# Performance work log

Measured on AMD Instinct MI355X. Metric: run time of the kernel, lower is better.

Reference implementation:

```python
import jax, jax.numpy as jnp
import numpy as np

N = 100000      # nodes
F_IN = 512      # num_features
H = 256         # hidden
C = 64          # num_classes
E = 3200000     # edges
K = 10          # APPNP propagation steps
ALPHA = 0.1     # teleport probability


def setup_inputs() -> dict:
    key = jax.random.key(0)
    k_x, k_w0, k_w1, k_e = jax.random.split(key, 4)
    x = jax.random.normal(k_x, (N, F_IN), dtype=jnp.float32)
    w0 = jax.random.normal(k_w0, (F_IN, H), dtype=jnp.float32) / np.sqrt(F_IN).astype(np.float32)
    b0 = jnp.zeros((H,), dtype=jnp.float32)
    w1 = jax.random.normal(k_w1, (H, C), dtype=jnp.float32) / np.sqrt(H).astype(np.float32)
    b1 = jnpps = jnp.zeros((C,), dtype=jnp.float32)
    edge_index = jax.random.randint(k_e, (2, E), 0, N, dtype=jnp.int64)
    return {"x": x, "w0": w0, "b0": b0, "w1": w1, "b1": b1, "edge_index": edge_index}


def _appnp(h, edge_index):
    # Add self loops (PyG APPNP default: gcn_norm with self loops).
    loops = jnp.arange(N, dtype=edge_index.dtype)
    src = jnp.concatenate([edge_index[0], loops])
    dst = jnp.concatenate([edge_index[1], loops])
    # Symmetric GCN normalization: D^{-1/2} (A+I) D^{-1/2}
    deg = jax.ops.segment_sum(jnp.ones_like(src, dtype=h.dtype), dst, num_segments=N)
    dinv = jnp.where(deg > 0, jax.lax.rsqrt(deg), 0.0)
    norm = dinv[src] * dinv[dst]  # [E+N]

    def step(xc, _):
        msg = norm[:, None] * xc[src]                      # gather [E+N, C]
        agg = jax.ops.segment_sum(msg, dst, num_segments=N)  # scatter-add [N, C]
        return (1.0 - ALPHA) * agg + ALPHA * h, None

    out, _ = jax.lax.scan(step, h, None, length=K)
    return out


def reference(x, w0, b0, w1, b1, edge_index):
    # eval mode: dropout is identity
    h = jax.nn.relu(x @ w0 + b0)   # [N, H]
    h = h @ w1 + b1                # [N, C]
    z = _appnp(h, edge_index)      # [N, C]
    return jax.nn.log_softmax(z, axis=1)
```

## Files before the change

kernel.cpp:

```cpp
#include <hip/hip_runtime.h>
#include <hip/hip_bf16.h>

#define NN 100000
#define EE 3200000
#define FIN 512
#define HH 256
#define CC 64
#define KSTEPS 10
#define SB 391
#define NBUC 782
#define EPB 16384
#define NEB 196

typedef __attribute__((ext_vector_type(8))) short bf16x8;
typedef __attribute__((ext_vector_type(8))) short s16x8;
typedef __attribute__((ext_vector_type(4))) float f32x4;
typedef unsigned short ushort_t;

__device__ __forceinline__ short f2bf(float f) {
    union { __hip_bfloat16 h; short s; } u;
    u.h = __float2bfloat16(f);
    return u.s;
}

__device__ __forceinline__ void glds16(const void* g, void* l) {
    __builtin_amdgcn_global_load_lds(
        (const __attribute__((address_space(1))) void*)g,
        (__attribute__((address_space(3))) void*)l, 16, 0, 0);
}

__global__ void prep_w(const float* __restrict__ w0, const float* __restrict__ w1,
                       short* __restrict__ w0t, short* __restrict__ w1t) {
    int t = blockIdx.x * blockDim.x + threadIdx.x;
    if (t < FIN * HH) {
        int k = t >> 8, n = t & 255;
        w0t[n * FIN + k] = f2bf(w0[t]);
    } else if (t < FIN * HH + HH * CC) {
        int u = t - FIN * HH;
        int k = u >> 6, n = u & 63;
        w1t[n * HH + k] = f2bf(w1[u]);
    }
}

__global__ __launch_bounds__(256) void bincnt(const int* __restrict__ ei,
                                              int* __restrict__ bcnt) {
    __shared__ int hb[NBUC];
    int tid = threadIdx.x;
    int base = blockIdx.x * EPB;
    for (int i = tid; i < NBUC; i += 256) hb[i] = 0;
    __syncthreads();
#pragma unroll 4
    for (int i = 0; i < EPB / 256; ++i) {
        int t = base + i * 256 + tid;
        if (t < EE) atomicAdd(&hb[(unsigned)ei[EE + t] >> 7], 1);
    }
    __syncthreads();
    for (int i = tid; i < NBUC; i += 256)
        if (hb[i]) atomicAdd(&bcnt[i], hb[i]);
}

__global__ __launch_bounds__(1024) void bscan(const int* __restrict__ bcnt,
                                              int* __restrict__ eboff) {
    __shared__ int sh[1024];
    int t = threadIdx.x;
    int v = (t < NBUC) ? bcnt[t] : 0;
    sh[t] = v;
    __syncthreads();
    for (int off = 1; off < 1024; off <<= 1) {
        int add = (t >= off) ? sh[t - off] : 0;
        __syncthreads();
        sh[t] += add;
        __syncthreads();
    }
    if (t < NBUC) eboff[t] = sh[t] - v;
}

__global__ __launch_bounds__(256) void binfill(const int* __restrict__ ei,
                                               const int* __restrict__ eboff,
                                               int* __restrict__ bfc,
                                               int* __restrict__ stg) {
    __shared__ int hb[NBUC];
    __shared__ int lb[NBUC];
    int tid = threadIdx.x;
    int base = blockIdx.x * EPB;
    for (int i = tid; i < NBUC; i += 256) hb[i] = 0;
    __syncthreads();
#pragma unroll 4
    for (int i = 0; i < EPB / 256; ++i) {
        int t = base + i * 256 + tid;
        if (t < EE) atomicAdd(&hb[(unsigned)ei[EE + t] >> 7], 1);
    }
    __syncthreads();
    for (int i = tid; i < NBUC; i += 256) {
        int c = hb[i];
        lb[i] = eboff[i] + (c ? atomicAdd(&bfc[i], c) : 0);
        hb[i] = 0;
    }
    __syncthreads();
#pragma unroll 4
    for (int i = 0; i < EPB / 256; ++i) {
        int t = base + i * 256 + tid;
        if (t < EE) {
            int s = ei[t];
            int d = ei[EE + t];
            int b = (unsigned)d >> 7;
            int o = atomicAdd(&hb[b], 1);
            stg[lb[b] + o] = (s << 7) | (d & 127);
        }
    }
}

__global__ __launch_bounds__(256) void bhist(const int* __restrict__ stg,
                                             const int* __restrict__ eboff,
                                             const int* __restrict__ bcnt,
                                             int* __restrict__ cnt) {
    __shared__ int nc[128];
    int b = blockIdx.x, tid = threadIdx.x;
    if (tid < 128) nc[tid] = 0;
    __syncthreads();
    int s0 = eboff[b], n = bcnt[b];
    for (int i = tid; i < n; i += 256) atomicAdd(&nc[stg[s0 + i] & 127], 1);
    __syncthreads();
    int node = b * 128 + tid;
    if (tid < 128 && node < NN) cnt[node] = nc[tid];
}

__global__ __launch_bounds__(256) void deg_kernel(const int* __restrict__ cnt,
                                                  float* __restrict__ dinv,
                                                  float* __restrict__ wco,
                                                  float* __restrict__ sdg,
                                                  int* __restrict__ bsum,
                                                  int* __restrict__ dbc) {
    __shared__ int red[256];
    __shared__ int h[64];
    int tid = threadIdx.x;
    if (tid < 64) h[tid] = 0;
    int i = blockIdx.x * 256 + tid;
    int d = 0, bin = 0;
    if (i < NN) {
        int c = cnt[i];
        d = c + 1;
        bin = min(c, 63);
        float fd = (float)d;
        dinv[i] = rsqrtf(fd);
        wco[i] = 0.9f / fd;
        sdg[i] = sqrtf(fd);
    }
    red[tid] = d;
    __syncthreads();
    if (i < NN) atomicAdd(&h[bin], 1);
    for (int off = 128; off > 0; off >>= 1) {
        if (tid < off) red[tid] += red[tid + off];
        __syncthreads();
    }
    if (tid == 0) bsum[blockIdx.x] = red[0];
    if (tid < 64 && h[tid]) atomicAdd(&dbc[tid], h[tid]);
}

__global__ __launch_bounds__(512) void scanb_kernel(const int* __restrict__ bsum,
                                                    int* __restrict__ boff,
                                                    const int* __restrict__ dbc,
                                                    int* __restrict__ dboff) {
    __shared__ int sh[512];
    int t = threadIdx.x;
    int v = (t < SB) ? bsum[t] : 0;
    sh[t] = v;
    __syncthreads();
    for (int off = 1; off < 512; off <<= 1) {
        int add = (t >= off) ? sh[t - off] : 0;
        __syncthreads();
        sh[t] += add;
        __syncthreads();
    }
    if (t < SB) boff[t] = sh[t] - v;
    __syncthreads();
    int v2 = (t < 64) ? dbc[t] : 0;
    __syncthreads();
    if (t < 64) sh[t] = v2;
    __syncthreads();
    for (int off = 1; off < 64; off <<= 1) {
        int add = (t >= off && t < 64) ? sh[t - off] : 0;
        __syncthreads();
        if (t < 64) sh[t] += add;
        __syncthreads();
    }
    if (t < 64) dboff[t] = sh[t] - v2;
}

__global__ __launch_bounds__(256) void rp_kernel(const int* __restrict__ cnt,
                                                 const int* __restrict__ boff,
                                                 int* __restrict__ rp) {
    __shared__ int sh[256];
    int i = blockIdx.x * 256 + threadIdx.x;
    int d = (i < NN) ? cnt[i] + 1 : 0;
    sh[threadIdx.x] = d;
    __syncthreads();
    for (int off = 1; off < 256; off <<= 1) {
        int add = (threadIdx.x >= off) ? sh[threadIdx.x - off] : 0;
        __syncthreads();
        sh[threadIdx.x] += add;
        __syncthreads();
    }
    int incl = sh[threadIdx.x];
    if (i < NN) rp[i] = boff[blockIdx.x] + incl - d;
    if (i == NN - 1) rp[NN] = boff[blockIdx.x] + incl;
}

__global__ __launch_bounds__(256) void bfill2(const int* __restrict__ stg,
                                              const int* __restrict__ eboff,
                                              const int* __restrict__ bcnt,
                                              const int* __restrict__ rp,
                                              int* __restrict__ eds) {
    __shared__ int nfc[128];
    __shared__ int rpl[129];
    int b = blockIdx.x, tid = threadIdx.x;
    int nodes = min(128, NN - b * 128);
    if (tid < 128) nfc[tid] = 0;
    if (tid <= 128) rpl[tid] = rp[min(b * 128 + tid, NN)];
    __syncthreads();
    int s0 = eboff[b], n = bcnt[b];
    for (int i = tid; i < n; i += 256) {
        int e = stg[s0 + i];
        int loc = e & 127;
        int o = atomicAdd(&nfc[loc], 1);
        eds[rpl[loc] + o] = e >> 7;
    }
    __syncthreads();
    if (tid < nodes) eds[rpl[tid + 1] - 1] = b * 128 + tid;
}

__global__ __launch_bounds__(256) void dperm(const int* __restrict__ cnt,
                                             const int* __restrict__ dboff,
                                             int* __restrict__ dfc,
                                             int* __restrict__ perm) {
    __shared__ int h[64];
    __shared__ int base[64];
    int tid = threadIdx.x;
    int i = blockIdx.x * 256 + tid;
    if (tid < 64) h[tid] = 0;
    __syncthreads();
    int bin = 0, r = 0;
    bool ok = i < NN;
    if (ok) {
        bin = min(cnt[i], 63);
        r = atomicAdd(&h[bin], 1);
    }
    __syncthreads();
    if (tid < 64) {
        int c = h[tid];
        base[tid] = dboff[tid] + (c ? atomicAdd(&dfc[tid], c) : 0);
    }
    __syncthreads();
    if (ok) perm[base[bin] + r] = i;
}

__global__ __launch_bounds__(256) void gemm1(const float* __restrict__ x,
                                             const short* __restrict__ w0t,
                                             const float* __restrict__ b0,
                                             short* __restrict__ h0) {
    __shared__ __align__(16) short As[128 * 64];
    __shared__ __align__(16) short Bs[2][128 * 64];
    const int tid = threadIdx.x;
    const int lane = tid & 63;
    const int wid = tid >> 6;
    const int wm = wid >> 1, wn = wid & 1;
    const int bn0 = blockIdx.x * 128;
    const long row0 = (long)blockIdx.y * 128;

    const int ar = tid >> 3;
    const int ako = tid & 7;
    const int aslot = ako ^ (ar & 7);
    const int cl = lane >> 3;
    const int bko = (lane & 7) ^ cl;

    float4 pa[4][2];

    auto loadA = [&](int kt) {
#pragma unroll
        for (int i = 0; i < 4; ++i) {
            long grow = row0 + i * 32 + ar;
            const float* src = x + grow * FIN + kt * 64 + ako * 8;
            if (grow < NN) {
                pa[i][0] = *(const float4*)src;
                pa[i][1] = *(const float4*)(src + 4);
            } else {
                pa[i][0] = make_float4(0.f, 0.f, 0.f, 0.f);
                pa[i][1] = make_float4(0.f, 0.f, 0.f, 0.f);
            }
        }
    };
    auto writeA = [&]() {
#pragma unroll
        for (int i = 0; i < 4; ++i) {
            int r = i * 32 + ar;
            s16x8 o;
            o[0] = f2bf(pa[i][0].x); o[1] = f2bf(pa[i][0].y);
            o[2] = f2bf(pa[i][0].z); o[3] = f2bf(pa[i][0].w);
            o[4] = f2bf(pa[i][1].x); o[5] = f2bf(pa[i][1].y);
            o[6] = f2bf(pa[i][1].z); o[7] = f2bf(pa[i][1].w);
            *(s16x8*)(&As[(r * 8 + aslot) * 8]) = o;
        }
    };
    auto stageB = [&](int kt, int buf) {
#pragma unroll
        for (int j = 0; j < 4; ++j) {
            int blk = wid * 4 + j;
            const short* g = w0t + (size_t)(bn0 + blk * 8 + cl) * FIN + kt * 64 + bko * 8;
            glds16(g, &Bs[buf][blk * 512]);
        }
    };

    f32x4 acc[4][4] = {};

    stageB(0, 0);
    loadA(0);
    writeA();
    __syncthreads();

    for (int kt = 0; kt < FIN / 64; ++kt) {
        int cur = kt & 1;
        if (kt < FIN / 64 - 1) {
            stageB(kt + 1, cur ^ 1);
            loadA(kt + 1);
        }
#pragma unroll
        for (int ks = 0; ks < 2; ++ks) {
            int ko = ks * 4 + (lane >> 4);
            int slot = ko ^ (lane & 7);
            bf16x8 af[4], bfr[4];
#pragma unroll
            for (int i = 0; i < 4; ++i) {
                int row = wm * 64 + i * 16 + (lane & 15);
                af[i] = *(const bf16x8*)(&As[(row * 8 + slot) * 8]);
            }
#pragma unroll
            for (int j = 0; j < 4; ++j) {
                int col = wn * 64 + j * 16 + (lane & 15);
                bfr[j] = *(const bf16x8*)(&Bs[cur][(col * 8 + slot) * 8]);
            }
#pragma unroll
            for (int i = 0; i < 4; ++i)
#pragma unroll
                for (int j = 0; j < 4; ++j)
                    acc[i][j] = __builtin_amdgcn_mfma_f32_16x16x32_bf16(af[i], bfr[j], acc[i][j], 0, 0, 0);
        }
        __syncthreads();
        if (kt < FIN / 64 - 1) writeA();
        __syncthreads();
    }
#pragma unroll
    for (int j = 0; j < 4; ++j) {
        int gcol = bn0 + wn * 64 + j * 16 + (lane & 15);
        float bias = b0[gcol];
#pragma unroll
        for (int i = 0; i < 4; ++i)
#pragma unroll
            for (int q = 0; q < 4; ++q) {
                long grow = row0 + wm * 64 + i * 16 + (lane >> 4) * 4 + q;
                float v = acc[i][j][q] + bias;
                if (v < 0.f) v = 0.f;
                h0[grow * HH + gcol] = f2bf(v);
            }
    }
}

__global__ __launch_bounds__(256) void gemm2(const short* __restrict__ h0,
                                             const short* __restrict__ w1t,
                                             const float* __restrict__ b1,
                                             const float* __restrict__ dinv,
                                             float* __restrict__ hv,
                                             ushort_t* __restrict__ v0) {
    __shared__ __align__(16) short As[2][128 * 64];
    __shared__ __align__(16) short Bs[2][64 * 64];
    const int tid = threadIdx.x;
    const int lane = tid & 63;
    const int wid = tid >> 6;
    const int wm = wid >> 1, wn = wid & 1;
    const long row0 = (long)blockIdx.x * 128;
    const int rl = lane >> 3;
    const int gko = (lane & 7) ^ rl;

    auto stage = [&](int kt, int buf) {
#pragma unroll
        for (int j = 0; j < 4; ++j) {
            int blk = wid * 4 + j;
            const short* g = h0 + (row0 + blk * 8 + rl) * HH + kt * 64 + gko * 8;
            glds16(g, &As[buf][blk * 512]);
        }
#pragma unroll
        for (int j = 0; j < 2; ++j) {
            int blk = wid * 2 + j;
            const short* g = w1t + (size_t)(blk * 8 + rl) * HH + kt * 64 + gko * 8;
            glds16(g, &Bs[buf][blk * 512]);
        }
    };

    f32x4 acc[4][2] = {};
    stage(0, 0);
    __syncthreads();
    for (int kt = 0; kt < HH / 64; ++kt) {
        int cur = kt & 1;
        if (kt < HH / 64 - 1) stage(kt + 1, cur ^ 1);
#pragma unroll
        for (int ks = 0; ks < 2; ++ks) {
            int ko = ks * 4 + (lane >> 4);
            int slot = ko ^ (lane & 7);
            bf16x8 af[4], bfr[2];
#pragma unroll
            for (int i = 0; i < 4; ++i) {
                int row = wm * 64 + i * 16 + (lane & 15);
                af[i] = *(const bf16x8*)(&As[cur][(row * 8 + slot) * 8]);
            }
#pragma unroll
            for (int j = 0; j < 2; ++j) {
                int col = wn * 32 + j * 16 + (lane & 15);
                bfr[j] = *(const bf16x8*)(&Bs[cur][(col * 8 + slot) * 8]);
            }
#pragma unroll
            for (int i = 0; i < 4; ++i)
#pragma unroll
                for (int j = 0; j < 2; ++j)
                    acc[i][j] = __builtin_amdgcn_mfma_f32_16x16x32_bf16(af[i], bfr[j], acc[i][j], 0, 0, 0);
        }
        __syncthreads();
    }
#pragma unroll
    for (int i = 0; i < 4; ++i)
#pragma unroll
        for (int j = 0; j < 2; ++j) {
            int col = wn * 32 + j * 16 + (lane & 15);
            float bias = b1[col];
#pragma unroll
            for (int q = 0; q < 4; ++q) {
                long grow = row0 + wm * 64 + i * 16 + (lane >> 4) * 4 + q;
                if (grow < NN) {
                    float hval = acc[i][j][q] + bias;
                    float dv = dinv[grow];
                    hv[grow * CC + col] = 0.1f * dv * hval;
                    v0[grow * CC + col] = (ushort_t)f2bf(dv * hval);
                }
            }
        }
}

__device__ __forceinline__ void gath(float a[8], const ushort_t* __restrict__ vin,
                                     int src, int l) {
    const int4 r = *(const int4*)(vin + ((size_t)src << 6) + (l << 3));
    a[0] += __int_as_float(r.x << 16);
    a[1] += __int_as_float(r.x & 0xffff0000);
    a[2] += __int_as_float(r.y << 16);
    a[3] += __int_as_float(r.y & 0xffff0000);
    a[4] += __int_as_float(r.z << 16);
    a[5] += __int_as_float(r.z & 0xffff0000);
    a[6] += __int_as_float(r.w << 16);
    a[7] += __int_as_float(r.w & 0xffff0000);
}

template <int LAST>
__global__ __launch_bounds__(256) void prop(const ushort_t* __restrict__ vin,
                                            const float* __restrict__ hv,
                                            const float* __restrict__ wco,
                                            const float* __restrict__ sdg,
                                            ushort_t* __restrict__ vout,
                                            float* __restrict__ zout,
                                            const int* __restrict__ rp,
                                            const int* __restrict__ eds,
                                            const int* __restrict__ perm) {
    int g = perm[blockIdx.x * 32 + (threadIdx.x >> 3)];
    int l = threadIdx.x & 7;
    int beg = rp[g], end = rp[g + 1];
    float a0[8] = {}, a1[8] = {}, a2[8] = {}, a3[8] = {};
    int e = beg;
    int head = (beg + 3) & ~3;
    if (head > end) head = end;
    for (; e < head; ++e) gath(a0, vin, eds[e], l);
    for (; e + 3 < end; e += 4) {
        int4 ee = *(const int4*)(eds + e);
        gath(a0, vin, ee.x, l);
        gath(a1, vin, ee.y, l);
        gath(a2, vin, ee.z, l);
        gath(a3, vin, ee.w, l);
    }
    for (; e < end; ++e) gath(a1, vin, eds[e], l);

    float w = wco[g];
    f32x4 hv0 = *(const f32x4*)(hv + ((size_t)g << 6) + (l << 3));
    f32x4 hv1 = *(const f32x4*)(hv + ((size_t)g << 6) + (l << 3) + 4);
    float r[8];
#pragma unroll
    for (int c = 0; c < 8; ++c)
        r[c] = w * ((a0[c] + a1[c]) + (a2[c] + a3[c])) + ((c < 4) ? hv0[c] : hv1[c - 4]);
    if (!LAST) {
        s16x8 o;
#pragma unroll
        for (int c = 0; c < 8; ++c) o[c] = f2bf(r[c]);
        *(s16x8*)(vout + ((size_t)g << 6) + (l << 3)) = o;
    } else {
        float sd = sdg[g];
#pragma unroll
        for (int c = 0; c < 8; ++c) r[c] *= sd;
        float m = r[0];
#pragma unroll
        for (int c = 1; c < 8; ++c) m = fmaxf(m, r[c]);
#pragma unroll
        for (int off = 1; off < 8; off <<= 1) m = fmaxf(m, __shfl_xor(m, off));
        float s = 0.f;
#pragma unroll
        for (int c = 0; c < 8; ++c) s += expf(r[c] - m);
#pragma unroll
        for (int off = 1; off < 8; off <<= 1) s += __shfl_xor(s, off);
        float ls = m + logf(s);
        f32x4 o0, o1;
#pragma unroll
        for (int c = 0; c < 4; ++c) { o0[c] = r[c] - ls; o1[c] = r[c + 4] - ls; }
        *(f32x4*)(zout + ((size_t)g << 6) + (l << 3)) = o0;
        *(f32x4*)(zout + ((size_t)g << 6) + (l << 3) + 4) = o1;
    }
}

extern "C" void kernel_launch(void* const* d_in, const int* in_sizes, int n_in,
                              void* d_out, int out_size, void* d_ws, size_t ws_size,
                              hipStream_t stream) {
    const float* x  = (const float*)d_in[0];
    const float* w0 = (const float*)d_in[1];
    const float* b0 = (const float*)d_in[2];
    const float* w1 = (const float*)d_in[3];
    const float* b1 = (const float*)d_in[4];
    const int*   ei = (const int*)d_in[5];

    char* ws = (char*)d_ws;
    size_t off = 0;
    auto take = [&](size_t n) { size_t r = off; off += (n + 255) & ~(size_t)255; return r; };
    size_t o_h0    = take((size_t)100096 * HH * 2);
    size_t o_vA    = take((size_t)NN * CC * 2);
    size_t o_hv    = take((size_t)NN * CC * 4);
    size_t o_ed    = take((size_t)(EE + NN) * 4);
    size_t o_rp    = take((size_t)(NN + 1) * 4);
    size_t o_cnt   = take((size_t)NN * 4);
    size_t o_dinv  = take((size_t)NN * 4);
    size_t o_wco   = take((size_t)NN * 4);
    size_t o_sdg   = take((size_t)NN * 4);
    size_t o_perm  = take((size_t)NN * 4);
    size_t o_w0t   = take((size_t)HH * FIN * 2);
    size_t o_w1t   = take((size_t)CC * HH * 2);
    size_t o_bs    = take((size_t)SB * 4);
    size_t o_bo    = take((size_t)SB * 4);
    size_t o_eboff = take((size_t)NBUC * 4);
    size_t o_dboff = take((size_t)64 * 4);
    size_t o_z     = take((size_t)(NBUC + NBUC + 64 + 64) * 4);

    short*    h0    = (short*)(ws + o_h0);
    ushort_t* vA    = (ushort_t*)(ws + o_vA);
    ushort_t* vB    = (ushort_t*)(ws + o_h0);
    float*    hv    = (float*)(ws + o_hv);
    int*      stg   = (int*)(ws + o_hv);
    int*      eds   = (int*)(ws + o_ed);
    int*      rp    = (int*)(ws + o_rp);
    int*      cnt   = (int*)(ws + o_cnt);
    float*    dinv  = (float*)(ws + o_dinv);
    float*    wco   = (float*)(ws + o_wco);
    float*    sdg   = (float*)(ws + o_sdg);
    int*      perm  = (int*)(ws + o_perm);
    short*    w0t   = (short*)(ws + o_w0t);
    short*    w1t   = (short*)(ws + o_w1t);
    int*      bs    = (int*)(ws + o_bs);
    int*      bo    = (int*)(ws + o_bo);
    int*      eboff = (int*)(ws + o_eboff);
    int*      dboff = (int*)(ws + o_dboff);
    int*      bcnt  = (int*)(ws + o_z);
    int*      bfc   = bcnt + NBUC;
    int*      dbc   = bfc + NBUC;
    int*      dfc   = dbc + 64;
    float*    zout  = (float*)d_out;

    prep_w<<<(FIN * HH + HH * CC + 255) / 256, 256, 0, stream>>>(w0, w1, w0t, w1t);
    hipMemsetAsync(ws + o_z, 0, (size_t)(NBUC + NBUC + 64 + 64) * 4, stream);

    bincnt<<<NEB, 256, 0, stream>>>(ei, bcnt);
    bscan<<<1, 1024, 0, stream>>>(bcnt, eboff);
    binfill<<<NEB, 256, 0, stream>>>(ei, eboff, bfc, stg);
    bhist<<<NBUC, 256, 0, stream>>>(stg, eboff, bcnt, cnt);
    deg_kernel<<<SB, 256, 0, stream>>>(cnt, dinv, wco, sdg, bs, dbc);
    scanb_kernel<<<1, 512, 0, stream>>>(bs, bo, dbc, dboff);
    rp_kernel<<<SB, 256, 0, stream>>>(cnt, bo, rp);
    bfill2<<<NBUC, 256, 0, stream>>>(stg, eboff, bcnt, rp, eds);
    dperm<<<SB, 256, 0, stream>>>(cnt, dboff, dfc, perm);

    gemm1<<<dim3(2, 782), 256, 0, stream>>>(x, w0t, b0, h0);
    gemm2<<<782, 256, 0, stream>>>(h0, w1t, b1, dinv, hv, vA);

    const ushort_t* in = vA;
    for (int k = 0; k < KSTEPS; ++k) {
        if (k == KSTEPS - 1) {
            prop<1><<<NN / 32, 256, 0, stream>>>(in, hv, wco, sdg, nullptr, zout, rp, eds, perm);
        } else {
            ushort_t* o = (k & 1) ? vA : vB;
            prop<0><<<NN / 32, 256, 0, stream>>>(in, hv, wco, sdg, o, nullptr, rp, eds, perm);
            in = o;
        }
    }
}
```

Measured before the change: 928.1 us.

## Pre-convert x to bf16 for async LDS staging and store teleport term in bf16

Adds a kernel that converts x to bf16 up front, letting gemm1 stage both operands with direct global-to-LDS loads and double buffering instead of register conversion. The teleport term hv is stored in bf16, halving its reads in every propagation step. The separate conversion pass adds a full extra read and write of x, and the smaller hv buffer shrinks the region aliased by the edge staging buffer.

```diff
diff --git a/kernel.cpp b/kernel.cpp
--- a/kernel.cpp
+++ b/kernel.cpp
@@ -39,6 +39,20 @@
         int u = t - FIN * HH;
         int k = u >> 6, n = u & 63;
         w1t[n * HH + k] = f2bf(w1[u]);
+    }
+}
+
+__global__ __launch_bounds__(256) void x2b_kernel(const float* __restrict__ x,
+                                                  ushort_t* __restrict__ xb) {
+    const long NTOT = (long)NN * FIN;
+    long stride = (long)gridDim.x * 256 * 8;
+    for (long i = ((long)blockIdx.x * 256 + threadIdx.x) * 8; i < NTOT; i += stride) {
+        float4 a = *(const float4*)(x + i);
+        float4 b = *(const float4*)(x + i + 4);
+        s16x8 o;
+        o[0] = f2bf(a.x); o[1] = f2bf(a.y); o[2] = f2bf(a.z); o[3] = f2bf(a.w);
+        o[4] = f2bf(b.x); o[5] = f2bf(b.y); o[6] = f2bf(b.z); o[7] = f2bf(b.w);
+        *(s16x8*)(xb + i) = o;
     }
 }
 
@@ -254,11 +268,11 @@
     if (ok) perm[base[bin] + r] = i;
 }
 
-__global__ __launch_bounds__(256) void gemm1(const float* __restrict__ x,
+__global__ __launch_bounds__(256) void gemm1(const ushort_t* __restrict__ xb,
                                              const short* __restrict__ w0t,
                                              const float* __restrict__ b0,
                                              short* __restrict__ h0) {
-    __shared__ __align__(16) short As[128 * 64];
+    __shared__ __align__(16) short As[2][128 * 64];
     __shared__ __align__(16) short Bs[2][128 * 64];
     const int tid = threadIdx.x;
     const int lane = tid & 63;
@@ -266,63 +280,30 @@
     const int wm = wid >> 1, wn = wid & 1;
     const int bn0 = blockIdx.x * 128;
     const long row0 = (long)blockIdx.y * 128;
-
-    const int ar = tid >> 3;
-    const int ako = tid & 7;
-    const int aslot = ako ^ (ar & 7);
-    const int cl = lane >> 3;
-    const int bko = (lane & 7) ^ cl;
-
-    float4 pa[4][2];
-
-    auto loadA = [&](int kt) {
-#pragma unroll
-        for (int i = 0; i < 4; ++i) {
-            long grow = row0 + i * 32 + ar;
-            const float* src = x + grow * FIN + kt * 64 + ako * 8;
-            if (grow < NN) {
-                pa[i][0] = *(const float4*)src;
-                pa[i][1] = *(const float4*)(src + 4);
-            } else {
-                pa[i][0] = make_float4(0.f, 0.f, 0.f, 0.f);
-                pa[i][1] = make_float4(0.f, 0.f, 0.f, 0.f);
-            }
-        }
-    };
-    auto writeA = [&]() {
-#pragma unroll
-        for (int i = 0; i < 4; ++i) {
-            int r = i * 32 + ar;
-            s16x8 o;
-            o[0] = f2bf(pa[i][0].x); o[1] = f2bf(pa[i][0].y);
-            o[2] = f2bf(pa[i][0].z); o[3] = f2bf(pa[i][0].w);
-            o[4] = f2bf(pa[i][1].x); o[5] = f2bf(pa[i][1].y);
-            o[6] = f2bf(pa[i][1].z); o[7] = f2bf(pa[i][1].w);
-            *(s16x8*)(&As[(r * 8 + aslot) * 8]) = o;
-        }
-    };
-    auto stageB = [&](int kt, int buf) {
+    const int rl = lane >> 3;
+    const int gko = (lane & 7) ^ rl;
+
+    auto stage = [&](int kt, int buf) {
 #pragma unroll
         for (int j = 0; j < 4; ++j) {
             int blk = wid * 4 + j;
-            const short* g = w0t + (size_t)(bn0 + blk * 8 + cl) * FIN + kt * 64 + bko * 8;
+            const ushort_t* g = xb + (row0 + blk * 8 + rl) * FIN + kt * 64 + gko * 8;
+            glds16(g, &As[buf][blk * 512]);
+        }
+#pragma unroll
+        for (int j = 0; j < 4; ++j) {
+            int blk = wid * 4 + j;
+            const short* g = w0t + (size_t)(bn0 + blk * 8 + rl) * FIN + kt * 64 + gko * 8;
             glds16(g, &Bs[buf][blk * 512]);
         }
     };
 
     f32x4 acc[4][4] = {};
-
-    stageB(0, 0);
-    loadA(0);
-    writeA();
-    __syncthreads();
-
+    stage(0, 0);
+    __syncthreads();
     for (int kt = 0; kt < FIN / 64; ++kt) {
         int cur = kt & 1;
-        if (kt < FIN / 64 - 1) {
-            stageB(kt + 1, cur ^ 1);
-            loadA(kt + 1);
-        }
+        if (kt < FIN / 64 - 1) stage(kt + 1, cur ^ 1);
 #pragma unroll
         for (int ks = 0; ks < 2; ++ks) {
             int ko = ks * 4 + (lane >> 4);
@@ -331,7 +312,7 @@
 #pragma unroll
             for (int i = 0; i < 4; ++i) {
                 int row = wm * 64 + i * 16 + (lane & 15);
-                af[i] = *(const bf16x8*)(&As[(row * 8 + slot) * 8]);
+                af[i] = *(const bf16x8*)(&As[cur][(row * 8 + slot) * 8]);
             }
 #pragma unroll
             for (int j = 0; j < 4; ++j) {
@@ -344,8 +325,6 @@
                 for (int j = 0; j < 4; ++j)
                     acc[i][j] = __builtin_amdgcn_mfma_f32_16x16x32_bf16(af[i], bfr[j], acc[i][j], 0, 0, 0);
         }
-        __syncthreads();
-        if (kt < FIN / 64 - 1) writeA();
         __syncthreads();
     }
 #pragma unroll
@@ -368,7 +347,7 @@
                                              const short* __restrict__ w1t,
                                              const float* __restrict__ b1,
                                              const float* __restrict__ dinv,
-                                             float* __restrict__ hv,
+                                             ushort_t* __restrict__ hvb,
                                              ushort_t* __restrict__ v0) {
     __shared__ __align__(16) short As[2][128 * 64];
     __shared__ __align__(16) short Bs[2][64 * 64];
@@ -436,7 +415,7 @@
                 if (grow < NN) {
                     float hval = acc[i][j][q] + bias;
                     float dv = dinv[grow];
-                    hv[grow * CC + col] = 0.1f * dv * hval;
+                    hvb[grow * CC + col] = (ushort_t)f2bf(0.1f * dv * hval);
                     v0[grow * CC + col] = (ushort_t)f2bf(dv * hval);
                 }
             }
@@ -458,7 +437,7 @@
 
 template <int LAST>
 __global__ __launch_bounds__(256) void prop(const ushort_t* __restrict__ vin,
-                                            const float* __restrict__ hv,
+                                            const ushort_t* __restrict__ hvb,
                                             const float* __restrict__ wco,
                                             const float* __restrict__ sdg,
                                             ushort_t* __restrict__ vout,
@@ -484,12 +463,20 @@
     for (; e < end; ++e) gath(a1, vin, eds[e], l);
 
     float w = wco[g];
-    f32x4 hv0 = *(const f32x4*)(hv + ((size_t)g << 6) + (l << 3));
-    f32x4 hv1 = *(const f32x4*)(hv + ((size_t)g << 6) + (l << 3) + 4);
+    const int4 hb = *(const int4*)(hvb + ((size_t)g << 6) + (l << 3));
+    float tv[8];
+    tv[0] = __int_as_float(hb.x << 16);
+    tv[1] = __int_as_float(hb.x & 0xffff0000);
+    tv[2] = __int_as_float(hb.y << 16);
+    tv[3] = __int_as_float(hb.y & 0xffff0000);
+    tv[4] = __int_as_float(hb.z << 16);
+    tv[5] = __int_as_float(hb.z & 0xffff0000);
+    tv[6] = __int_as_float(hb.w << 16);
+    tv[7] = __int_as_float(hb.w & 0xffff0000);
     float r[8];
 #pragma unroll
     for (int c = 0; c < 8; ++c)
-        r[c] = w * ((a0[c] + a1[c]) + (a2[c] + a3[c])) + ((c < 4) ? hv0[c] : hv1[c - 4]);
+        r[c] = w * ((a0[c] + a1[c]) + (a2[c] + a3[c])) + tv[c];
     if (!LAST) {
         s16x8 o;
 #pragma unroll
@@ -533,7 +520,7 @@
     auto take = [&](size_t n) { size_t r = off; off += (n + 255) & ~(size_t)255; return r; };
     size_t o_h0    = take((size_t)100096 * HH * 2);
     size_t o_vA    = take((size_t)NN * CC * 2);
-    size_t o_hv    = take((size_t)NN * CC * 4);
+    size_t o_hv    = take((size_t)NN * CC * 2);
     size_t o_ed    = take((size_t)(EE + NN) * 4);
     size_t o_rp    = take((size_t)(NN + 1) * 4);
     size_t o_cnt   = take((size_t)NN * 4);
@@ -548,11 +535,12 @@
     size_t o_eboff = take((size_t)NBUC * 4);
     size_t o_dboff = take((size_t)64 * 4);
     size_t o_z     = take((size_t)(NBUC + NBUC + 64 + 64) * 4);
+    size_t o_xb    = take((size_t)100096 * FIN * 2);
 
     short*    h0    = (short*)(ws + o_h0);
     ushort_t* vA    = (ushort_t*)(ws + o_vA);
     ushort_t* vB    = (ushort_t*)(ws + o_h0);
-    float*    hv    = (float*)(ws + o_hv);
+    ushort_t* hvb   = (ushort_t*)(ws + o_hv);
     int*      stg   = (int*)(ws + o_hv);
     int*      eds   = (int*)(ws + o_ed);
     int*      rp    = (int*)(ws + o_rp);
@@ -571,6 +559,7 @@
     int*      bfc   = bcnt + NBUC;
     int*      dbc   = bfc + NBUC;
     int*      dfc   = dbc + 64;
+    ushort_t* xb    = (ushort_t*)(ws + o_xb);
     float*    zout  = (float*)d_out;
 
     prep_w<<<(FIN * HH + HH * CC + 255) / 256, 256, 0, stream>>>(w0, w1, w0t, w1t);
@@ -586,16 +575,17 @@
     bfill2<<<NBUC, 256, 0, stream>>>(stg, eboff, bcnt, rp, eds);
     dperm<<<SB, 256, 0, stream>>>(cnt, dboff, dfc, perm);
 
-    gemm1<<<dim3(2, 782), 256, 0, stream>>>(x, w0t, b0, h0);
-    gemm2<<<782, 256, 0, stream>>>(h0, w1t, b1, dinv, hv, vA);
+    x2b_kernel<<<2048, 256, 0, stream>>>(x, xb);
+    gemm1<<<dim3(2, 782), 256, 0, stream>>>(xb, w0t, b0, h0);
+    gemm2<<<782, 256, 0, stream>>>(h0, w1t, b1, dinv, hvb, vA);
 
     const ushort_t* in = vA;
     for (int k = 0; k < KSTEPS; ++k) {
         if (k == KSTEPS - 1) {
-            prop<1><<<NN / 32, 256, 0, stream>>>(in, hv, wco, sdg, nullptr, zout, rp, eds, perm);
+            prop<1><<<NN / 32, 256, 0, stream>>>(in, hvb, wco, sdg, nullptr, zout, rp, eds, perm);
         } else {
             ushort_t* o = (k & 1) ? vA : vB;
-            prop<0><<<NN / 32, 256, 0, stream>>>(in, hv, wco, sdg, o, nullptr, rp, eds, perm);
+            prop<0><<<NN / 32, 256, 0, stream>>>(in, hvb, wco, sdg, o, nullptr, rp, eds, perm);
             in = o;
         }
     }
```

Result: no change. 930.9 us (+0.3%).
